# Performance work log

Hardware: AMD Instinct MI355X
Metric: run time of the kernel (lower is better)

## Reference

```python
import jax, jax.numpy as jnp
import numpy as np

B, C, H, W = 2, 48, 128, 256
HEADS = 3
EPS_LN = 1e-6
EPS_NRM = 1e-12


def _conv(x, w, b, padding=0, dilation=1, groups=1):
    # x: NCHW, w: OIHW
    out = jax.lax.conv_general_dilated(
        x, w, window_strides=(1, 1),
        padding=[(padding, padding), (padding, padding)],
        rhs_dilation=(dilation, dilation),
        feature_group_count=groups,
        dimension_numbers=('NCHW', 'OIHW', 'NCHW'))
    return out + b[None, :, None, None]


def _ln2d(x, w, b):
    # LayerNorm over channel dim per pixel (NAFNet-style LayerNorm2d)
    mu = x.mean(axis=1, keepdims=True)
    var = ((x - mu) ** 2).mean(axis=1, keepdims=True)
    return (x - mu) / jnp.sqrt(var + EPS_LN) * w[None, :, None, None] + b[None, :, None, None]


def _l2norm(x):
    # F.normalize(dim=-1): x / max(||x||_2, eps)
    n = jnp.sqrt((x * x).sum(-1, keepdims=True))
    return x / jnp.maximum(n, EPS_NRM)


def setup_inputs() -> dict:
    key = jax.random.key(0)
    ks = iter(jax.random.split(key, 40))
    def nrm(shape, s=0.02):
        return jax.random.normal(next(ks), shape, jnp.float32) * s
    d = {
        'x_l': jax.random.normal(next(ks), (B, C, H, W), jnp.float32),
        'x_r': jax.random.normal(next(ks), (B, C, H, W), jnp.float32),
        'ln1_w': jnp.ones((C,), jnp.float32), 'ln1_b': jnp.zeros((C,), jnp.float32),
        'ln2_w': jnp.ones((C,), jnp.float32), 'ln2_b': jnp.zeros((C,), jnp.float32),
        'qkv_l_w': nrm((3 * C, C, 1, 1)), 'qkv_l_b': jnp.zeros((3 * C,), jnp.float32),
        'qkv_r_w': nrm((3 * C, C, 1, 1)), 'qkv_r_b': jnp.zeros((3 * C,), jnp.float32),
        'dw_l_w': nrm((3 * C, 1, 3, 3)), 'dw_l_b': jnp.zeros((3 * C,), jnp.float32),
        'dw_r_w': nrm((3 * C, 1, 3, 3)), 'dw_r_b': jnp.zeros((3 * C,), jnp.float32),
        'dil0_w': nrm((2 * C, 2 * C, 3, 3)), 'dil0_b': jnp.zeros((2 * C,), jnp.float32),
        'dil1_w': nrm((2 * C, 2 * C, 3, 3)), 'dil1_b': jnp.zeros((2 * C,), jnp.float32),
        'dil2_w': nrm((2 * C, 2 * C, 3, 3)), 'dil2_b': jnp.zeros((2 * C,), jnp.float32),
        'convQ_w': nrm((C, 6 * C, 1, 1)), 'convQ_b': jnp.zeros((C,), jnp.float32),
        'conv1_w': nrm((C, C, 1, 1)), 'conv1_b': jnp.zeros((C,), jnp.float32),
        'conv2_w': nrm((C, C, 1, 1)), 'conv2_b': jnp.zeros((C,), jnp.float32),
        'temperature': jnp.ones((HEADS, 1, 1), jnp.float32),
    }
    return d


def reference(x_l, x_r, ln1_w, ln1_b, ln2_w, ln2_b,
              qkv_l_w, qkv_l_b, qkv_r_w, qkv_r_b,
              dw_l_w, dw_l_b, dw_r_w, dw_r_b,
              dil0_w, dil0_b, dil1_w, dil1_b, dil2_w, dil2_b,
              convQ_w, convQ_b, conv1_w, conv1_b, conv2_w, conv2_b,
              temperature):
    b, c, h, w = x_l.shape
    hw = h * w
    ch = c // HEADS  # channels per head

    norm_l = _ln2d(x_l, ln1_w, ln1_b)
    norm_r = _ln2d(x_r, ln2_w, ln2_b)

    qkvl = _conv(_conv(norm_l, qkv_l_w, qkv_l_b), dw_l_w, dw_l_b, padding=1, groups=3 * c)
    qkvr = _conv(_conv(norm_r, qkv_r_w, qkv_r_b), dw_r_w, dw_r_b, padding=1, groups=3 * c)
    Q_l, K_l, V_l = jnp.split(qkvl, 3, axis=1)
    Q_r, K_r, V_r = jnp.split(qkvr, 3, axis=1)

    Q = jnp.concatenate((Q_l, Q_r), axis=1)  # [b, 2c, h, w]
    Q = jnp.concatenate((
        _conv(Q, dil0_w, dil0_b, padding=2, dilation=2),
        _conv(Q, dil1_w, dil1_b, padding=4, dilation=4),
        _conv(Q, dil2_w, dil2_b, padding=6, dilation=6)), axis=1)  # [b, 6c, h, w]
    Q = _conv(Q, convQ_w, convQ_b)  # [b, c, h, w]

    def heads(t):
        return t.reshape(b, HEADS, ch, hw)

    Q = _l2norm(heads(Q))
    K_l = _l2norm(heads(K_l))
    K_r = _l2norm(heads(K_r))
    V_l = heads(V_l)
    V_r = heads(V_r)

    # channel attention: [b, head, ch, ch]
    A_r2l = jax.nn.softmax(jnp.einsum('bhcn,bhdn->bhcd', Q, K_r) * temperature, axis=-1)
    A_l2r = jax.nn.softmax(jnp.einsum('bhcn,bhdn->bhcd', Q, K_l) * temperature, axis=-1)

    F_l = jnp.einsum('bhcd,bhdn->bhcn', A_r2l, V_l).reshape(b, c, h, w)
    F_r = jnp.einsum('bhcd,bhdn->bhcn', A_l2r, V_r).reshape(b, c, h, w)

    F_l = _conv(F_l, conv1_w, conv1_b)
    F_r = _conv(F_r, conv2_w, conv2_b)
    return (x_l + F_l, x_r + F_r)
```

## Files before the change

### kernel.cpp

```cpp
#include <hip/hip_runtime.h>
#include <hip/hip_bf16.h>

typedef __hip_bfloat16 bf16;
typedef __attribute__((ext_vector_type(8))) short short8;
typedef __attribute__((ext_vector_type(4))) float f32x4;

constexpr int IMG_H = 128;
constexpr int IMG_W = 256;
constexpr int HW    = IMG_H * IMG_W;
constexpr int BB    = 2;
constexpr int CC    = 48;
constexpr int C3    = 144;
constexpr int XPW   = 268;
constexpr int XOFF  = 6;

constexpr int WO_QKVL_W = 0;
constexpr int WO_QKVR_W = 6912;
constexpr int WO_DWL_W  = 13824;
constexpr int WO_DWR_W  = 15120;
constexpr int WO_C1_W   = 16416;
constexpr int WO_C2_W   = 18720;
constexpr int WO_QKVL_B = 21024;
constexpr int WO_QKVR_B = 21168;
constexpr int WO_DWL_B  = 21312;
constexpr int WO_DWR_B  = 21456;
constexpr int WO_C1_B   = 21600;
constexpr int WO_C2_B   = 21648;
constexpr int WO_LN1W   = 21696;
constexpr int WO_LN1B   = 21744;
constexpr int WO_LN2W   = 21792;
constexpr int WO_LN2B   = 21840;
constexpr int WO_TEMP   = 21888;
constexpr int WO_WQ     = 21952;
constexpr int WO_D0W    = 35776;
constexpr int WO_D1W    = 118720;
constexpr int WO_D2W    = 201664;
constexpr int WO_BQ     = 284608;
constexpr int WO_B0     = 284656;
constexpr int WO_B1     = 284752;
constexpr int WO_B2     = 284848;
constexpr int WO_WPACK  = 284944;
constexpr int WO_EFFB   = 409360;
constexpr int WO_NQ     = 409424;
constexpr int WO_NKL    = 409520;
constexpr int WO_NKR    = 409616;
constexpr int WO_AR2L   = 409712;
constexpr int WO_AL2R   = 411248;
constexpr int WO_M1     = 412800;
constexpr int WO_M2     = 417408;
constexpr int WO_WQP    = 422016;
constexpr int WO_PART   = 431232;

constexpr size_t ACT_BASE_BYTES = 2118144;

constexpr size_t A_P  = 0;
constexpr size_t A_Q1 = 9437184;
constexpr size_t A_Q2 = 18874368;
constexpr size_t A_QC = 28311552;

struct PrepArgs {
  const void* src[25];
  int dst[25];
  int n[25];
};

__device__ __forceinline__ bool probe_bf16(const void* ln1w) {
  return ((const unsigned short*)ln1w)[0] == 0x3F80;
}

__global__ __launch_bounds__(256) void prep_k(PrepArgs a, float* __restrict__ wsf) {
  bool isb = probe_bf16(a.src[12]);
  int t = blockIdx.y;
  int i = blockIdx.x * 256 + threadIdx.x;
  if (i < a.n[t]) {
    float v = isb ? __bfloat162float(((const bf16*)a.src[t])[i])
                  : ((const float*)a.src[t])[i];
    wsf[a.dst[t] + i] = v;
  }
}

__global__ __launch_bounds__(256) void effw2_k(const float* __restrict__ wsf,
                                               bf16* __restrict__ wpack) {
  int d  = blockIdx.x / 96;
  int ci = blockIdx.x % 96;
  __shared__ float wds[864];
  __shared__ float wqs[48 * 97];
  const int wdb = (d == 0) ? WO_D0W : (d == 1) ? WO_D1W : WO_D2W;
  for (int idx = threadIdx.x; idx < 864; idx += 256) {
    int m = idx / 9, tt = idx % 9;
    wds[idx] = wsf[wdb + (m * 96 + ci) * 9 + tt];
  }
  for (int idx = threadIdx.x; idx < 4608; idx += 256) {
    int co = idx / 96, m = idx % 96;
    wqs[co * 97 + m] = wsf[WO_WQ + co * 288 + d * 96 + m];
  }
  __syncthreads();
  int tco = threadIdx.x;
  if (tco < 432) {
    int t = tco / 48, co = tco % 48;
    float s = 0.f;
#pragma unroll 8
    for (int m = 0; m < 96; ++m) s += wqs[co * 97 + m] * wds[m * 9 + t];
    int trow = t / 3, dxi = t % 3;
    int ti = (trow == 0) ? (2 - d) * 3 + dxi
           : (trow == 1) ? 9 + d * 3 + dxi
                         : 18 + d * 3 + dxi;
    int kc = ci >> 5, j = ci & 7;
    int L = ((ci & 31) >> 3) * 16 + (co & 15);
    int nt = co >> 4;
    int f = (ti * 3 + kc) * 3 + nt;
    wpack[(size_t)f * 512 + L * 8 + j] = __float2bfloat16(s);
  }
}

__global__ __launch_bounds__(64) void effb_k(const float* __restrict__ wsf,
                                             float* __restrict__ effb) {
  int co = threadIdx.x;
  if (co >= 48) return;
  float s = wsf[WO_BQ + co];
  for (int m = 0; m < 96; ++m) {
    s += wsf[WO_WQ + co * 288 + m]       * wsf[WO_B0 + m];
    s += wsf[WO_WQ + co * 288 + 96 + m]  * wsf[WO_B1 + m];
    s += wsf[WO_WQ + co * 288 + 192 + m] * wsf[WO_B2 + m];
  }
  effb[co] = s;
}

__global__ __launch_bounds__(256) void wqp_k(const float* __restrict__ wsf,
                                             bf16* __restrict__ wqp) {
  int idx = blockIdx.x * 256 + threadIdx.x;
  if (idx >= 18432) return;
  int side = idx / 9216;
  int rem = idx % 9216;
  int nt = rem / 1024;
  int kt = (rem / 512) % 2;
  int e  = rem % 512;
  int L = e >> 3, j = e & 7;
  int o = nt * 16 + (L & 15);
  int kp = kt * 32 + (L >> 4) * 8 + j;
  int g = kp >> 4, r = kp & 15;
  float val = 0.f;
  if (r < 12) {
    int c = g * 12 + r;
    val = wsf[(side ? WO_QKVR_W : WO_QKVL_W) + o * 48 + c];
  }
  wqp[idx] = __float2bfloat16(val);
}

__global__ __launch_bounds__(256) void lnqkv_k(
    const void* __restrict__ x, const void* __restrict__ probe,
    const float* __restrict__ lnw, const float* __restrict__ lnb,
    const bf16* __restrict__ wqp_side, const float* __restrict__ qb,
    bf16* __restrict__ pre) {
  __shared__ __align__(16) unsigned char LDSU[21504 + 18432];
  bf16* XNs = (bf16*)LDSU;
  float2* red = (float2*)(LDSU + 9216);
  bf16* Cs = (bf16*)LDSU;
  bf16* W = (bf16*)(LDSU + 21504);
  int tid = threadIdx.x;
  for (int i = tid; i < 1152; i += 256)
    ((uint4*)W)[i] = ((const uint4*)wqp_side)[i];

  int px = tid & 63;
  int w = tid >> 6;
  int p = blockIdx.x * 64 + px;
  int b = p >> 15;
  int pix = p & (HW - 1);
  size_t base = (size_t)b * CC * HW + pix;
  float v[12];
  if (probe_bf16(probe)) {
    const bf16* xp = (const bf16*)x + base;
#pragma unroll
    for (int c = 0; c < 12; ++c)
      v[c] = __bfloat162float(xp[(size_t)(w * 12 + c) * HW]);
  } else {
    const float* xp = (const float*)x + base;
#pragma unroll
    for (int c = 0; c < 12; ++c) v[c] = xp[(size_t)(w * 12 + c) * HW];
  }
  float s = 0.f, s2 = 0.f;
#pragma unroll
  for (int c = 0; c < 12; ++c) { s += v[c]; s2 += v[c] * v[c]; }
  red[w * 64 + px] = make_float2(s, s2);
  __syncthreads();
  float S = 0.f, S2 = 0.f;
#pragma unroll
  for (int i = 0; i < 4; ++i) {
    float2 r2 = red[i * 64 + px];
    S += r2.x; S2 += r2.y;
  }
  float mu = S * (1.f / 48.f);
  float var = S2 * (1.f / 48.f) - mu * mu;
  float rs = rsqrtf(var + 1e-6f);
  bf16 o16[16];
#pragma unroll
  for (int c = 0; c < 12; ++c)
    o16[c] = __float2bfloat16((v[c] - mu) * rs * lnw[w * 12 + c] + lnb[w * 12 + c]);
#pragma unroll
  for (int c = 12; c < 16; ++c) o16[c] = __float2bfloat16(0.f);
  *(uint4*)(XNs + px * 72 + w * 16) = *(uint4*)(o16);
  *(uint4*)(XNs + px * 72 + w * 16 + 8) = *(uint4*)(o16 + 8);
  __syncthreads();

  int L = tid & 63;
  int lo = L & 15, hi = L >> 4;
  const bf16* arow = XNs + (size_t)(w * 16 + lo) * 72 + hi * 8;
  short8 a0 = *(const short8*)(arow);
  short8 a1 = *(const short8*)(arow + 32);
  __syncthreads();
#pragma unroll
  for (int nt = 0; nt < 9; ++nt) {
    float bvv = qb[nt * 16 + lo];
    f32x4 acc = {bvv, bvv, bvv, bvv};
    acc = __builtin_amdgcn_mfma_f32_16x16x32_bf16(
        a0, *(const short8*)(W + (nt * 2 + 0) * 512 + L * 8), acc, 0, 0, 0);
    acc = __builtin_amdgcn_mfma_f32_16x16x32_bf16(
        a1, *(const short8*)(W + (nt * 2 + 1) * 512 + L * 8), acc, 0, 0, 0);
#pragma unroll
    for (int r = 0; r < 4; ++r)
      Cs[(nt * 16 + lo) * 66 + w * 16 + hi * 4 + r] = __float2bfloat16(acc[r]);
  }
  __syncthreads();
  int pix0 = (blockIdx.x * 64) & (HW - 1);
#pragma unroll
  for (int pass = 0; pass < 18; ++pass) {
    int o = pass * 8 + (tid >> 5);
    int px2 = (tid & 31) * 2;
    bf16 t2[2];
    t2[0] = Cs[o * 66 + px2];
    t2[1] = Cs[o * 66 + px2 + 1];
    *(unsigned*)(pre + ((size_t)(b * C3 + o)) * HW + pix0 + px2) = *(unsigned*)t2;
  }
}

__global__ __launch_bounds__(256) void dw_k(
    const bf16* __restrict__ in, const float* __restrict__ w9,
    const float* __restrict__ bias, bf16* __restrict__ out) {
  int gid = blockIdx.x;
  int yt = gid & 15;
  int c = (gid >> 4) % C3;
  int b = gid / (16 * C3);
  int ry = threadIdx.x >> 5, xi = threadIdx.x & 31;
  int y = yt * 8 + ry;
  int x0 = xi * 8;
  const bf16* base = in + ((size_t)(b * C3 + c)) * HW;
  float wv[9];
#pragma unroll
  for (int t = 0; t < 9; ++t) wv[t] = w9[c * 9 + t];
  float bz = bias[c];
  float acc[8];
#pragma unroll
  for (int i = 0; i < 8; ++i) acc[i] = bz;
#pragma unroll
  for (int ky = 0; ky < 3; ++ky) {
    int yy = y + ky - 1;
    if ((unsigned)yy >= (unsigned)IMG_H) continue;
    const bf16* row = base + yy * IMG_W + x0;
    uint4 m = *(const uint4*)(row);
    float f[10];
    f[0] = (x0 > 0) ? __bfloat162float(row[-1]) : 0.f;
    f[9] = (x0 + 8 < IMG_W) ? __bfloat162float(row[8]) : 0.f;
    f[1] = __uint_as_float(m.x << 16);
    f[2] = __uint_as_float(m.x & 0xFFFF0000u);
    f[3] = __uint_as_float(m.y << 16);
    f[4] = __uint_as_float(m.y & 0xFFFF0000u);
    f[5] = __uint_as_float(m.z << 16);
    f[6] = __uint_as_float(m.z & 0xFFFF0000u);
    f[7] = __uint_as_float(m.w << 16);
    f[8] = __uint_as_float(m.w & 0xFFFF0000u);
    float w0 = wv[ky * 3], w1 = wv[ky * 3 + 1], w2 = wv[ky * 3 + 2];
#pragma unroll
    for (int i = 0; i < 8; ++i)
      acc[i] += w0 * f[i] + w1 * f[i + 1] + w2 * f[i + 2];
  }
  bf16 o[8];
#pragma unroll
  for (int i = 0; i < 8; ++i) o[i] = __float2bfloat16(acc[i]);
  *(uint4*)(out + ((size_t)(b * C3 + c)) * HW + y * IMG_W + x0) = *(uint4*)o;
}

__global__ __launch_bounds__(256) void qc_k(const bf16* __restrict__ q1,
                                            const bf16* __restrict__ q2,
                                            bf16* __restrict__ qc) {
  int b = blockIdx.x >> 7;
  int y = blockIdx.x & 127;
  int half = blockIdx.y;
  int tid = threadIdx.x;
  int x0 = half * 128;
  int px = tid & 127;
  int cig = tid >> 7;
  __shared__ __align__(16) bf16 T[128][100];
#pragma unroll 8
  for (int k = 0; k < 48; ++k) {
    int ci = cig * 48 + k;
    const bf16* src = (ci < 48)
        ? q1 + (((size_t)(b * C3 + ci)) * IMG_H + y) * IMG_W
        : q2 + (((size_t)(b * C3 + ci - 48)) * IMG_H + y) * IMG_W;
    T[px][ci] = src[x0 + px];
  }
  __syncthreads();
  size_t rowbase = ((size_t)(b * IMG_H + y)) * XPW * 96 + (size_t)half * 12864;
#pragma unroll 1
  for (int i = 0; i < 13; ++i) {
    int e4 = i * 256 + tid;
    if (e4 >= 3216) break;
    int e = e4 * 4;
    int xp = (e + half * 12864) / 96;
    int ci = (e + half * 12864) % 96;
    int x = xp - XOFF;
    uint2 val;
    if ((unsigned)x < (unsigned)IMG_W) {
      val = *(const uint2*)(&T[x - x0][ci]);
    } else {
      val.x = 0u; val.y = 0u;
    }
    *(uint2*)(qc + rowbase + e) = val;
  }
}

__global__ __launch_bounds__(256) void dil_mfma_k(
    const bf16* __restrict__ qc, const bf16* __restrict__ wp,
    const float* __restrict__ effb, bf16* __restrict__ qh) {
  __shared__ __align__(16) unsigned char LDSU[18432];
  bf16* Wb = (bf16*)LDSU;
  float* Cs = (float*)LDSU;
  int bid = blockIdx.x;
  int xcd = bid & 7;
  int slot = bid >> 3;
  int y = xcd * 16 + (slot & 15);
  int rest = slot >> 4;
  int xt = rest & 3;
  int b = rest >> 2;
  int x0 = xt * 64;
  int tid = threadIdx.x;
  int L = tid & 63;
  int w = tid >> 6;
  int lo = L & 15, hi = L >> 4;

  f32x4 acc[3];
#pragma unroll
  for (int nt = 0; nt < 3; ++nt) {
    float bv = effb[nt * 16 + lo];
    acc[nt] = {bv, bv, bv, bv};
  }
  const size_t abase =
      ((size_t)(b * IMG_H + y) * XPW + XOFF + x0 + w * 16 + lo) * 96 + hi * 8;

  {
    const uint4* src = (const uint4*)(wp);
    uint4* dst = (uint4*)(Wb);
    dst[tid] = src[tid];
    dst[tid + 256] = src[tid + 256];
    if (tid < 64) dst[tid + 512] = src[tid + 512];
  }
  __syncthreads();

#pragma unroll 1
  for (int ti = 0; ti < 27; ++ti) {
    if (ti + 1 < 27) {
      const uint4* src = (const uint4*)(wp + (ti + 1) * 4608);
      uint4* dst = (uint4*)(Wb + ((ti + 1) & 1) * 4608);
      dst[tid] = src[tid];
      dst[tid + 256] = src[tid + 256];
      if (tid < 64) dst[tid + 512] = src[tid + 512];
    }
    int g = ti / 3, dxi = ti - g * 3;
    int D = (g < 3) ? (6 - 2 * g) : (g < 6) ? (2 * (g - 2)) : (2 * (g - 5));
    int dy = (g < 3) ? -D : (g < 6) ? 0 : D;
    int dx = (dxi - 1) * D;
    if ((unsigned)(y + dy) < (unsigned)IMG_H) {
      const bf16* wb = Wb + (ti & 1) * 4608;
      const bf16* ap = qc + abase + ((long)dy * XPW + dx) * 96;
#pragma unroll
      for (int kc = 0; kc < 3; ++kc) {
        short8 a = *(const short8*)(ap + kc * 32);
        const bf16* wk = wb + kc * 3 * 512 + L * 8;
#pragma unroll
        for (int nt = 0; nt < 3; ++nt) {
          acc[nt] = __builtin_amdgcn_mfma_f32_16x16x32_bf16(
              a, *(const short8*)(wk + nt * 512), acc[nt], 0, 0, 0);
        }
      }
    }
    __syncthreads();
  }

#pragma unroll
  for (int nt = 0; nt < 3; ++nt)
#pragma unroll
    for (int r = 0; r < 4; ++r)
      Cs[(nt * 16 + lo) * 68 + w * 16 + hi * 4 + r] = acc[nt][r];
  __syncthreads();
#pragma unroll
  for (int i = 0; i < 3; ++i) {
    int e4 = i * 256 + tid;
    int co = e4 >> 4;
    int px4 = (e4 & 15) * 4;
    const float* srcp = &Cs[co * 68 + px4];
    bf16 tmp[4];
    tmp[0] = __float2bfloat16(srcp[0]);
    tmp[1] = __float2bfloat16(srcp[1]);
    tmp[2] = __float2bfloat16(srcp[2]);
    tmp[3] = __float2bfloat16(srcp[3]);
    *(uint2*)(qh + (((size_t)(b * CC + co)) * IMG_H + y) * IMG_W + x0 + px4) =
        *(uint2*)tmp;
  }
}

__device__ __forceinline__ float wave_sum(float v) {
#pragma unroll
  for (int off = 32; off > 0; off >>= 1) v += __shfl_down(v, off, 64);
  return v;
}

__device__ __forceinline__ float blo(unsigned u) {
  return __uint_as_float(u << 16);
}
__device__ __forceinline__ float bhi(unsigned u) {
  return __uint_as_float(u & 0xFFFF0000u);
}

__global__ __launch_bounds__(256) void rownorm_k(
    const bf16* __restrict__ qh, const bf16* __restrict__ qkvl,
    const bf16* __restrict__ qkvr, float* __restrict__ nq,
    float* __restrict__ nkl, float* __restrict__ nkr) {
  int id = blockIdx.x;
  int which = id / 96;
  int rid = id % 96;
  int b = rid / 48;
  int c = rid % 48;
  const bf16* ptr = (which == 0) ? qh + ((size_t)(b * CC + c)) * HW
                  : (which == 1) ? qkvl + ((size_t)(b * C3 + 48 + c)) * HW
                                 : qkvr + ((size_t)(b * C3 + 48 + c)) * HW;
  float s = 0.f;
#pragma unroll 2
  for (int it = 0; it < 16; ++it) {
    int n0 = (it * 256 + threadIdx.x) * 8;
    uint4 u = *(const uint4*)(ptr + n0);
    float a0 = blo(u.x), a1 = bhi(u.x), a2 = blo(u.y), a3 = bhi(u.y);
    float a4 = blo(u.z), a5 = bhi(u.z), a6 = blo(u.w), a7 = bhi(u.w);
    s += a0 * a0 + a1 * a1 + a2 * a2 + a3 * a3 + a4 * a4 + a5 * a5 +
         a6 * a6 + a7 * a7;
  }
  s = wave_sum(s);
  __shared__ float red[4];
  if ((threadIdx.x & 63) == 0) red[threadIdx.x >> 6] = s;
  __syncthreads();
  if (threadIdx.x == 0) {
    float tot = red[0] + red[1] + red[2] + red[3];
    float* dst = (which == 0) ? nq : (which == 1) ? nkl : nkr;
    dst[rid] = tot;
  }
}

__global__ __launch_bounds__(256) void logits_mfma_k(
    const bf16* __restrict__ qh, const bf16* __restrict__ qkvl,
    const bf16* __restrict__ qkvr, float* __restrict__ part) {
  int abh = blockIdx.x;
  int chunk = blockIdx.y;
  int a = abh / 6;
  int b = (abh / 3) % 2;
  int h = abh % 3;
  int tid = threadIdx.x;
  int L = tid & 63, w = tid >> 6;
  int lo = L & 15, hi = L >> 4;
  const bf16* qrow = qh + ((size_t)(b * CC + h * 16 + lo)) * HW;
  const bf16* krow =
      ((a == 0) ? qkvr : qkvl) + ((size_t)(b * C3 + 48 + h * 16 + lo)) * HW;
  int px0 = chunk * 1024 + w * 256 + hi * 8;
  f32x4 acc = {0.f, 0.f, 0.f, 0.f};
#pragma unroll
  for (int s = 0; s < 8; ++s) {
    short8 av = *(const short8*)(qrow + px0 + s * 32);
    short8 bv = *(const short8*)(krow + px0 + s * 32);
    acc = __builtin_amdgcn_mfma_f32_16x16x32_bf16(av, bv, acc, 0, 0, 0);
  }
  __shared__ float red[4][256];
#pragma unroll
  for (int r = 0; r < 4; ++r) red[w][(hi * 4 + r) * 16 + lo] = acc[r];
  __syncthreads();
  float sum = red[0][tid] + red[1][tid] + red[2][tid] + red[3][tid];
  part[((size_t)abh * 32 + chunk) * 256 + tid] = sum;
}

__global__ __launch_bounds__(256) void logits_red_k(
    const float* __restrict__ part, const float* __restrict__ nq,
    const float* __restrict__ nkl, const float* __restrict__ nkr,
    const float* __restrict__ temp, float* __restrict__ logr2l,
    float* __restrict__ logl2r) {
  int abh = blockIdx.x;
  int a = abh / 6, b = (abh / 3) % 2, h = abh % 3;
  int t = threadIdx.x;
  int i = t >> 4, j = t & 15;
  float s = 0.f;
  const float* p = part + (size_t)abh * 32 * 256 + t;
#pragma unroll 8
  for (int c = 0; c < 32; ++c) s += p[c * 256];
  float qn = fmaxf(sqrtf(nq[b * 48 + h * 16 + i]), 1e-12f);
  float kn = fmaxf(sqrtf(((a == 0) ? nkr : nkl)[b * 48 + h * 16 + j]), 1e-12f);
  float val = s / (qn * kn) * temp[h];
  ((a == 0) ? logr2l : logl2r)[b * 768 + h * 256 + i * 16 + j] = val;
}

__global__ __launch_bounds__(256) void softmaxM_k(float* __restrict__ wsf) {
  int tid = threadIdx.x;
  __shared__ float A1[1536], A2[1536];
  if (tid < 192) {
    const float* p = wsf + ((tid < 96) ? WO_AR2L : WO_AL2R) + (tid % 96) * 16;
    float* dst = ((tid < 96) ? A1 : A2) + (tid % 96) * 16;
    float m = -1e30f;
#pragma unroll
    for (int j = 0; j < 16; ++j) m = fmaxf(m, p[j]);
    float s = 0.f;
    float e[16];
#pragma unroll
    for (int j = 0; j < 16; ++j) {
      e[j] = expf(p[j] - m);
      s += e[j];
    }
    float inv = 1.f / s;
#pragma unroll
    for (int j = 0; j < 16; ++j) dst[j] = e[j] * inv;
  }
  __syncthreads();
#pragma unroll 1
  for (int idx = tid; idx < 4608; idx += 256) {
    int b = idx / 2304;
    int r = idx % 2304;
    int o = r / 48;
    int cp = r % 48;
    int h = cp >> 4, j = cp & 15;
    const float* a1 = &A1[((b * 3 + h) * 16) * 16 + j];
    const float* a2 = &A2[((b * 3 + h) * 16) * 16 + j];
    float s1 = 0.f, s2 = 0.f;
#pragma unroll
    for (int i = 0; i < 16; ++i) {
      s1 += wsf[WO_C1_W + o * 48 + h * 16 + i] * a1[i * 16];
      s2 += wsf[WO_C2_W + o * 48 + h * 16 + i] * a2[i * 16];
    }
    wsf[WO_M1 + idx] = s1;
    wsf[WO_M2 + idx] = s2;
  }
}

__global__ __launch_bounds__(256) void attn_out2_k(
    const bf16* __restrict__ q1, const bf16* __restrict__ q2,
    const void* __restrict__ x1, const void* __restrict__ x2,
    const void* __restrict__ probe, const float* __restrict__ Mall,
    const float* __restrict__ cball, void* __restrict__ out) {
  int side = blockIdx.z;
  const bf16* qkv = side ? q2 : q1;
  const void* x = side ? x2 : x1;
  const float* M = Mall + side * 4608;
  const float* cb = cball + side * 48;
  int tid = threadIdx.x;
  int p = blockIdx.x * 256 + tid;
  int b = __builtin_amdgcn_readfirstlane(p >> 15);
  int pix = p & (HW - 1);
  int o0 = blockIdx.y * 16;
  bool isb = probe_bf16(probe);

  float v[CC];
  const bf16* vb = qkv + ((size_t)(b * C3 + 96)) * HW + pix;
#pragma unroll
  for (int c = 0; c < CC; ++c) v[c] = __bfloat162float(vb[(size_t)c * HW]);

  const float* Mb = M + b * 2304;
  size_t base = (size_t)b * CC * HW + pix;
  float res[16];
#pragma unroll 2
  for (int o = 0; o < 16; ++o) {
    float acc = cb[o0 + o];
    const float* mrow = Mb + (o0 + o) * 48;
#pragma unroll
    for (int c = 0; c < CC; ++c) acc += mrow[c] * v[c];
    res[o] = acc;
  }
  size_t obase = (size_t)side * BB * CC * HW + base + (size_t)o0 * HW;
  if (isb) {
    const bf16* xp = (const bf16*)x + base + (size_t)o0 * HW;
    bf16* op = (bf16*)out + obase;
#pragma unroll
    for (int o = 0; o < 16; ++o)
      op[(size_t)o * HW] =
          __float2bfloat16(res[o] + __bfloat162float(xp[(size_t)o * HW]));
  } else {
    const float* xp = (const float*)x + base + (size_t)o0 * HW;
    float* op = (float*)out + obase;
#pragma unroll
    for (int o = 0; o < 16; ++o) op[(size_t)o * HW] = res[o] + xp[(size_t)o * HW];
  }
}

extern "C" void kernel_launch(void* const* d_in, const int* in_sizes, int n_in,
                              void* d_out, int out_size, void* d_ws, size_t ws_size,
                              hipStream_t stream) {
  (void)in_sizes; (void)n_in; (void)out_size; (void)ws_size;
  const void* x_l = d_in[0];
  const void* x_r = d_in[1];
  const void* probe = d_in[2];
  float* wsf = (float*)d_ws;
  bf16* wpack = (bf16*)(wsf + WO_WPACK);
  bf16* wqp = (bf16*)(wsf + WO_WQP);
  bf16* act = (bf16*)((char*)d_ws + ACT_BASE_BYTES);
  bf16* P  = act + A_P;
  bf16* Q1 = act + A_Q1;
  bf16* Q2 = act + A_Q2;
  bf16* QC = act + A_QC;
  bf16* qh = P;

  PrepArgs pa;
  const int srcIdx[25] = {6, 8, 10, 12, 22, 24, 7, 9, 11, 13, 23, 25,
                          2, 3, 4, 5, 26, 20, 14, 16, 18, 21, 15, 17, 19};
  const int dstOff[25] = {WO_QKVL_W, WO_QKVR_W, WO_DWL_W, WO_DWR_W, WO_C1_W, WO_C2_W,
                          WO_QKVL_B, WO_QKVR_B, WO_DWL_B, WO_DWR_B, WO_C1_B, WO_C2_B,
                          WO_LN1W, WO_LN1B, WO_LN2W, WO_LN2B, WO_TEMP,
                          WO_WQ, WO_D0W, WO_D1W, WO_D2W, WO_BQ, WO_B0, WO_B1, WO_B2};
  const int ns[25] = {6912, 6912, 1296, 1296, 2304, 2304, 144, 144, 144, 144,
                      48, 48, 48, 48, 48, 48, 3,
                      13824, 82944, 82944, 82944, 48, 96, 96, 96};
  for (int i = 0; i < 25; ++i) {
    pa.src[i] = d_in[srcIdx[i]];
    pa.dst[i] = dstOff[i];
    pa.n[i] = ns[i];
  }
  prep_k<<<dim3(324, 25), 256, 0, stream>>>(pa, wsf);

  effw2_k<<<288, 256, 0, stream>>>(wsf, wpack);
  effb_k<<<1, 64, 0, stream>>>(wsf, wsf + WO_EFFB);
  wqp_k<<<72, 256, 0, stream>>>(wsf, wqp);

  lnqkv_k<<<1024, 256, 0, stream>>>(x_l, probe, wsf + WO_LN1W, wsf + WO_LN1B,
                                    wqp, wsf + WO_QKVL_B, P);
  dw_k<<<BB * C3 * 16, 256, 0, stream>>>(P, wsf + WO_DWL_W, wsf + WO_DWL_B, Q1);
  lnqkv_k<<<1024, 256, 0, stream>>>(x_r, probe, wsf + WO_LN2W, wsf + WO_LN2B,
                                    wqp + 9216, wsf + WO_QKVR_B, P);
  dw_k<<<BB * C3 * 16, 256, 0, stream>>>(P, wsf + WO_DWR_W, wsf + WO_DWR_B, Q2);

  qc_k<<<dim3(BB * IMG_H, 2), 256, 0, stream>>>(Q1, Q2, QC);

  dil_mfma_k<<<1024, 256, 0, stream>>>(QC, wpack, wsf + WO_EFFB, qh);

  rownorm_k<<<288, 256, 0, stream>>>(qh, Q1, Q2, wsf + WO_NQ,
                                     wsf + WO_NKL, wsf + WO_NKR);
  logits_mfma_k<<<dim3(12, 32), 256, 0, stream>>>(qh, Q1, Q2, wsf + WO_PART);
  logits_red_k<<<12, 256, 0, stream>>>(wsf + WO_PART, wsf + WO_NQ,
                                       wsf + WO_NKL, wsf + WO_NKR,
                                       wsf + WO_TEMP, wsf + WO_AR2L,
                                       wsf + WO_AL2R);
  softmaxM_k<<<1, 256, 0, stream>>>(wsf);

  attn_out2_k<<<dim3(256, 3, 2), 256, 0, stream>>>(
      Q1, Q2, x_l, x_r, probe, wsf + WO_M1, wsf + WO_C1_B, d_out);
}
```

Before: 280.8 us.

## Stage full input rows in LDS and process whole image row per dilated-conv block

The dilated MFMA conv now gives each block a full 256-pixel output row instead of a 64-pixel tile, so the grid shrinks from 1024 to 256 blocks. For each distinct vertical offset, the block stages the padded input row once in LDS and reuses it across the three horizontal taps. Weight fragments are prefetched into registers and held while four pixel groups run MFMAs, giving four times more reuse of each weight load. Separately, effw2_k is launched with 512 threads so all 432 (tap, channel) outputs are computed. That second change corrects a previously incomplete weight fold. The trade-off is about 74 KB of LDS and one block per CU, which lowers occupancy and the ability to hide latency.

```diff
diff --git a/kernel.cpp b/kernel.cpp
--- a/kernel.cpp
+++ b/kernel.cpp
@@ -79,18 +79,18 @@
   }
 }
 
-__global__ __launch_bounds__(256) void effw2_k(const float* __restrict__ wsf,
+__global__ __launch_bounds__(512) void effw2_k(const float* __restrict__ wsf,
                                                bf16* __restrict__ wpack) {
   int d  = blockIdx.x / 96;
   int ci = blockIdx.x % 96;
   __shared__ float wds[864];
   __shared__ float wqs[48 * 97];
   const int wdb = (d == 0) ? WO_D0W : (d == 1) ? WO_D1W : WO_D2W;
-  for (int idx = threadIdx.x; idx < 864; idx += 256) {
+  for (int idx = threadIdx.x; idx < 864; idx += 512) {
     int m = idx / 9, tt = idx % 9;
     wds[idx] = wsf[wdb + (m * 96 + ci) * 9 + tt];
   }
-  for (int idx = threadIdx.x; idx < 4608; idx += 256) {
+  for (int idx = threadIdx.x; idx < 4608; idx += 512) {
     int co = idx / 96, m = idx % 96;
     wqs[co * 97 + m] = wsf[WO_WQ + co * 288 + d * 96 + m];
   }
@@ -318,92 +318,129 @@
   }
 }
 
-__global__ __launch_bounds__(256) void dil_mfma_k(
+__global__ __launch_bounds__(256, 1) void dil_mfma_k(
     const bf16* __restrict__ qc, const bf16* __restrict__ wp,
     const float* __restrict__ effb, bf16* __restrict__ qh) {
-  __shared__ __align__(16) unsigned char LDSU[18432];
-  bf16* Wb = (bf16*)LDSU;
-  float* Cs = (float*)LDSU;
+  __shared__ __align__(16) unsigned char LDSU[74176];
+  bf16* Arow = (bf16*)LDSU;
+  bf16* Wb   = (bf16*)(LDSU + 55744);
+  float* Cs  = (float*)LDSU;
+
   int bid = blockIdx.x;
   int xcd = bid & 7;
   int slot = bid >> 3;
   int y = xcd * 16 + (slot & 15);
-  int rest = slot >> 4;
-  int xt = rest & 3;
-  int b = rest >> 2;
-  int x0 = xt * 64;
+  int b = slot >> 4;
   int tid = threadIdx.x;
   int L = tid & 63;
   int w = tid >> 6;
   int lo = L & 15, hi = L >> 4;
 
-  f32x4 acc[3];
-#pragma unroll
-  for (int nt = 0; nt < 3; ++nt) {
-    float bv = effb[nt * 16 + lo];
-    acc[nt] = {bv, bv, bv, bv};
-  }
-  const size_t abase =
-      ((size_t)(b * IMG_H + y) * XPW + XOFF + x0 + w * 16 + lo) * 96 + hi * 8;
+  f32x4 acc[4][3];
+#pragma unroll
+  for (int g2 = 0; g2 < 4; ++g2)
+#pragma unroll
+    for (int nt = 0; nt < 3; ++nt) {
+      float bv = effb[nt * 16 + lo];
+      acc[g2][nt] = {bv, bv, bv, bv};
+    }
 
   {
-    const uint4* src = (const uint4*)(wp);
-    uint4* dst = (uint4*)(Wb);
-    dst[tid] = src[tid];
-    dst[tid + 256] = src[tid + 256];
-    if (tid < 64) dst[tid + 512] = src[tid + 512];
-  }
-  __syncthreads();
-
+    const uint4* ws = (const uint4*)wp;
+    uint4* wd = (uint4*)Wb;
+    wd[tid] = ws[tid];
+    wd[tid + 256] = ws[tid + 256];
+    if (tid < 64) wd[tid + 512] = ws[tid + 512];
+  }
+
+  int dy_prev = -100;
 #pragma unroll 1
-  for (int ti = 0; ti < 27; ++ti) {
-    if (ti + 1 < 27) {
-      const uint4* src = (const uint4*)(wp + (ti + 1) * 4608);
-      uint4* dst = (uint4*)(Wb + ((ti + 1) & 1) * 4608);
-      dst[tid] = src[tid];
-      dst[tid + 256] = src[tid + 256];
-      if (tid < 64) dst[tid + 512] = src[tid + 512];
-    }
-    int g = ti / 3, dxi = ti - g * 3;
+  for (int g = 0; g < 9; ++g) {
     int D = (g < 3) ? (6 - 2 * g) : (g < 6) ? (2 * (g - 2)) : (2 * (g - 5));
     int dy = (g < 3) ? -D : (g < 6) ? 0 : D;
-    int dx = (dxi - 1) * D;
-    if ((unsigned)(y + dy) < (unsigned)IMG_H) {
-      const bf16* wb = Wb + (ti & 1) * 4608;
-      const bf16* ap = qc + abase + ((long)dy * XPW + dx) * 96;
-#pragma unroll
-      for (int kc = 0; kc < 3; ++kc) {
-        short8 a = *(const short8*)(ap + kc * 32);
-        const bf16* wk = wb + kc * 3 * 512 + L * 8;
-#pragma unroll
-        for (int nt = 0; nt < 3; ++nt) {
-          acc[nt] = __builtin_amdgcn_mfma_f32_16x16x32_bf16(
-              a, *(const short8*)(wk + nt * 512), acc[nt], 0, 0, 0);
+    int yy = y + dy;
+    bool valid = (unsigned)yy < (unsigned)IMG_H;
+    if (valid && dy != dy_prev) {
+      const uint4* src = (const uint4*)(qc + (size_t)(b * IMG_H + yy) * (XPW * 96));
+      uint4 abuf[13];
+#pragma unroll
+      for (int r = 0; r < 13; ++r) {
+        int i = tid + r * 256;
+        if (i < 3216) abuf[r] = src[i];
+      }
+      __syncthreads();
+#pragma unroll
+      for (int r = 0; r < 13; ++r) {
+        int i = tid + r * 256;
+        if (i < 3216) {
+          int px = i / 12;
+          int cr = i - px * 12;
+          *(uint4*)(Arow + px * 104 + cr * 8) = abuf[r];
         }
       }
     }
-    __syncthreads();
-  }
-
-#pragma unroll
-  for (int nt = 0; nt < 3; ++nt)
-#pragma unroll
-    for (int r = 0; r < 4; ++r)
-      Cs[(nt * 16 + lo) * 68 + w * 16 + hi * 4 + r] = acc[nt][r];
-  __syncthreads();
-#pragma unroll
-  for (int i = 0; i < 3; ++i) {
-    int e4 = i * 256 + tid;
-    int co = e4 >> 4;
-    int px4 = (e4 & 15) * 4;
-    const float* srcp = &Cs[co * 68 + px4];
-    bf16 tmp[4];
-    tmp[0] = __float2bfloat16(srcp[0]);
-    tmp[1] = __float2bfloat16(srcp[1]);
-    tmp[2] = __float2bfloat16(srcp[2]);
-    tmp[3] = __float2bfloat16(srcp[3]);
-    *(uint2*)(qh + (((size_t)(b * CC + co)) * IMG_H + y) * IMG_W + x0 + px4) =
-        *(uint2*)tmp;
+    dy_prev = dy;
+#pragma unroll 1
+    for (int dxi = 0; dxi < 3; ++dxi) {
+      int ti = g * 3 + dxi;
+      uint4 w0, w1, w2;
+      if (ti < 26) {
+        const uint4* ws = (const uint4*)(wp + (ti + 1) * 4608);
+        w0 = ws[tid];
+        w1 = ws[tid + 256];
+        if (tid < 64) w2 = ws[tid + 512];
+      }
+      __syncthreads();
+      if (valid) {
+        const bf16* wb = Wb + (ti & 1) * 4608;
+        short8 bfr[9];
+#pragma unroll
+        for (int f = 0; f < 9; ++f)
+          bfr[f] = *(const short8*)(wb + f * 512 + L * 8);
+        int dx = (dxi - 1) * D;
+        const bf16* ar = Arow + (XOFF + dx + w * 64 + lo) * 104 + hi * 8;
+#pragma unroll
+        for (int g2 = 0; g2 < 4; ++g2)
+#pragma unroll
+          for (int kc = 0; kc < 3; ++kc) {
+            short8 a = *(const short8*)(ar + g2 * (16 * 104) + kc * 32);
+#pragma unroll
+            for (int nt = 0; nt < 3; ++nt)
+              acc[g2][nt] = __builtin_amdgcn_mfma_f32_16x16x32_bf16(
+                  a, bfr[kc * 3 + nt], acc[g2][nt], 0, 0, 0);
+          }
+      }
+      if (ti < 26) {
+        uint4* wd = (uint4*)(Wb + ((ti + 1) & 1) * 4608);
+        wd[tid] = w0;
+        wd[tid + 256] = w1;
+        if (tid < 64) wd[tid + 512] = w2;
+      }
+    }
+  }
+
+  __syncthreads();
+#pragma unroll
+  for (int g2 = 0; g2 < 4; ++g2)
+#pragma unroll
+    for (int nt = 0; nt < 3; ++nt)
+#pragma unroll
+      for (int r = 0; r < 4; ++r)
+        Cs[(nt * 16 + lo) * 260 + w * 64 + g2 * 16 + hi * 4 + r] = acc[g2][nt][r];
+  __syncthreads();
+  size_t obase = (size_t)b * CC * HW + (size_t)y * IMG_W;
+#pragma unroll 1
+  for (int i = 0; i < 12; ++i) {
+    int chunk = i * 256 + tid;
+    int co = chunk >> 6;
+    int px4 = (chunk & 63) * 4;
+    const float* s = Cs + co * 260 + px4;
+    bf16 t4[4];
+    t4[0] = __float2bfloat16(s[0]);
+    t4[1] = __float2bfloat16(s[1]);
+    t4[2] = __float2bfloat16(s[2]);
+    t4[3] = __float2bfloat16(s[3]);
+    *(uint2*)(qh + obase + (size_t)co * HW + px4) = *(uint2*)t4;
   }
 }
 
@@ -626,7 +663,7 @@
   }
   prep_k<<<dim3(324, 25), 256, 0, stream>>>(pa, wsf);
 
-  effw2_k<<<288, 256, 0, stream>>>(wsf, wpack);
+  effw2_k<<<288, 512, 0, stream>>>(wsf, wpack);
   effb_k<<<1, 64, 0, stream>>>(wsf, wsf + WO_EFFB);
   wqp_k<<<72, 256, 0, stream>>>(wsf, wqp);
 
@@ -639,7 +676,7 @@
 
   qc_k<<<dim3(BB * IMG_H, 2), 256, 0, stream>>>(Q1, Q2, QC);
 
-  dil_mfma_k<<<1024, 256, 0, stream>>>(QC, wpack, wsf + WO_EFFB, qh);
+  dil_mfma_k<<<256, 256, 0, stream>>>(QC, wpack, wsf + WO_EFFB, qh);
 
   rownorm_k<<<288, 256, 0, stream>>>(qh, Q1, Q2, wsf + WO_NQ,
                                      wsf + WO_NKL, wsf + WO_NKR);
```

Result: slower. 300.3 us (+7.0%).
